# Kernel tuning notes

Measured on AMD Instinct MI355X. Metric: run time of the kernel, lower is better.

## Reference

```python
import jax, jax.numpy as jnp
import numpy as np

B, T, C = 4, 2048, 2048
H, HKV, D = 16, 8, 128
SECTIONS = (24, 20, 20)  # sums to 64 = D/2 -> full-dim rotation branch
EPS = 1e-6


def setup_inputs() -> dict:
    key = jax.random.key(0)
    ks = jax.random.split(key, 8)
    x = jax.random.normal(ks[0], (B, T, C), dtype=jnp.float32)
    # realistic RoPE tables: [3, B, T, 64] (3 mRoPE axes: t/h/w)
    half = sum(SECTIONS)  # 64
    inv_freq = 1.0 / (10000.0 ** (jnp.arange(half, dtype=jnp.float32) / half))
    pos = jnp.arange(T, dtype=jnp.float32)
    freqs = pos[:, None] * inv_freq[None, :]                      # [T, 64]
    freqs3 = jnp.broadcast_to(freqs, (3, B, T, half))
    # small per-axis offsets so the three mRoPE axes differ
    axis_off = jnp.arange(3, dtype=jnp.float32)[:, None, None, None] * 0.5
    cos = jnp.cos(freqs3 + axis_off)
    sin = jnp.sin(freqs3 + axis_off)
    mask = jnp.ones((B, T), dtype=jnp.int32)
    s = 1.0 / np.sqrt(C)
    Wq = jax.random.normal(ks[1], (C, H * D), dtype=jnp.float32) * s
    Wk = jax.random.normal(ks[2], (C, HKV * D), dtype=jnp.float32) * s
    Wv = jax.random.normal(ks[3], (C, HKV * D), dtype=jnp.float32) * s
    Wo = jax.random.normal(ks[4], (H * D, C), dtype=jnp.float32) * (1.0 / np.sqrt(H * D))
    return dict(x=x, cos=cos, sin=sin, mask=mask,
                Wq=Wq, bq=jnp.zeros((H * D,), jnp.float32),
                Wk=Wk, bk=jnp.zeros((HKV * D,), jnp.float32),
                Wv=Wv, bv=jnp.zeros((HKV * D,), jnp.float32),
                gq=jnp.ones((D,), jnp.float32), gk=jnp.ones((D,), jnp.float32),
                Wo=Wo)


def _rms_norm(x, gamma, eps):
    var = jnp.mean(jnp.square(x.astype(jnp.float32)), axis=-1, keepdims=True)
    return (gamma * x * jax.lax.rsqrt(var + eps)).astype(x.dtype)


def _rotate_half(x):
    x1, x2 = jnp.split(x, 2, axis=-1)
    return jnp.concatenate((-x2, x1), axis=-1)


def _reorder(table):
    # interleave mRoPE sections: take section i from axis i, then duplicate
    chunks, off = [], 0
    for i, sec in enumerate(SECTIONS):
        chunks.append(table[i, ..., off:off + sec])
        off += sec
    r = jnp.concatenate(chunks, axis=-1)        # [B, T, 64]
    return jnp.concatenate([r, r], axis=-1)     # [B, T, 128]


def reference(x, cos, sin, mask, Wq, bq, Wk, bk, Wv, bv, gq, gk, Wo):
    b, t = x.shape[0], x.shape[1]
    q = (x @ Wq + bq).reshape(b, t, H, D)
    k = (x @ Wk + bk).reshape(b, t, HKV, D)
    v = (x @ Wv + bv).reshape(b, t, HKV, D)
    q = _rms_norm(q, gq, EPS)
    k = _rms_norm(k, gk, EPS)
    q = jnp.transpose(q, (0, 2, 1, 3))   # [B, H, T, D]
    k = jnp.transpose(k, (0, 2, 1, 3))   # [B, HKV, T, D]
    v = jnp.transpose(v, (0, 2, 1, 3))
    cos_e = _reorder(cos)[:, None].astype(q.dtype)  # [B, 1, T, D]
    sin_e = _reorder(sin)[:, None].astype(q.dtype)
    q = q * cos_e + _rotate_half(q) * sin_e
    k = k * cos_e + _rotate_half(k) * sin_e
    key_mask = mask.astype(jnp.float32)                         # [B, T]
    lengths = key_mask.sum(axis=-1).astype(jnp.int32)           # [B]
    k = k * key_mask[:, None, :, None].astype(k.dtype)
    v = v * key_mask[:, None, :, None].astype(v.dtype)
    history_mask = (jnp.arange(t)[None, :] < lengths[:, None]).astype(jnp.float32)
    repeats = H // HKV
    qg = q.reshape(b, HKV, repeats, t, D)
    scores = jnp.einsum('bhgqd,bhkd->bhgqk', qg.astype(jnp.float32),
                        k.astype(jnp.float32)) * D ** -0.5
    scores = scores.reshape(b, H, t, t)
    scores = scores + (1.0 - history_mask)[:, None, None, :] * -1e9
    causal = jnp.tril(jnp.ones((t, t), dtype=jnp.float32))
    scores = scores + (1.0 - causal)[None, None] * -1e9
    weights = jax.nn.softmax(scores, axis=-1)
    wg = weights.reshape(b, HKV, repeats, t, t)
    out = jnp.einsum('bhgqk,bhkd->bhgqd', wg, v.astype(jnp.float32))
    out = out.reshape(b, H, t, D).astype(x.dtype)
    out = jnp.transpose(out, (0, 2, 1, 3)).reshape(b, t, H * D)
    return out @ Wo
```

## Files before the change

### kernel.cpp

```cpp
#include <hip/hip_runtime.h>
#include <stdint.h>

#define B_    4
#define T_    2048
#define C_    2048
#define H_    16
#define HKV_  8
#define D_    128
#define HD_   2048
#define KVD_  1024
#define NQKV_ 4096
#define BT_   8192

typedef __bf16 bf16x8 __attribute__((ext_vector_type(8)));
typedef float  f32x4  __attribute__((ext_vector_type(4)));
typedef unsigned short u16;
typedef unsigned int   u32;

__device__ __forceinline__ u16 f2b(float f){
  union { float f; u32 u; } v; v.f = f;
  u32 r = v.u + 0x7FFFu + ((v.u >> 16) & 1u);
  return (u16)(r >> 16);
}
__device__ __forceinline__ float b2f(u16 h){
  union { u32 u; float f; } v; v.u = ((u32)h) << 16;
  return v.f;
}

#define GLOAD16(src, dst) __builtin_amdgcn_global_load_lds( \
    (const __attribute__((address_space(1))) u32*)(src), \
    (__attribute__((address_space(3))) u32*)(dst), 16, 0, 0)

#define MFMA16(a,b,c) __builtin_amdgcn_mfma_f32_16x16x32_bf16((a), (b), (c), 0, 0, 0)

__global__ __launch_bounds__(256) void k_misc(const float* __restrict__ x, u16* __restrict__ xb,
                                              const float* __restrict__ bq, const float* __restrict__ bk,
                                              const float* __restrict__ bv, float* __restrict__ bias,
                                              const int* __restrict__ mask, int* __restrict__ lens){
  int bid = blockIdx.x;
  if (bid < 16384){
    size_t i = ((size_t)bid * 256 + threadIdx.x) * 4;
    float4 v = *(const float4*)(x + i);
    u32 w0 = (u32)f2b(v.x) | ((u32)f2b(v.y) << 16);
    u32 w1 = (u32)f2b(v.z) | ((u32)f2b(v.w) << 16);
    uint2 pk; pk.x = w0; pk.y = w1;
    *(uint2*)(xb + i) = pk;
  } else if (bid < 16400){
    int i = (bid - 16384) * 256 + threadIdx.x;
    if (i < NQKV_)
      bias[i] = (i < HD_) ? bq[i] : (i < HD_ + KVD_ ? bk[i - HD_] : bv[i - HD_ - KVD_]);
  } else {
    int b = bid - 16400;
    int s = 0;
    for (int t = threadIdx.x; t < T_; t += 256) s += mask[b * T_ + t];
    #pragma unroll
    for (int d = 1; d < 64; d <<= 1) s += __shfl_xor(s, d);
    __shared__ int acc[4];
    if ((threadIdx.x & 63) == 0) acc[threadIdx.x >> 6] = s;
    __syncthreads();
    if (threadIdx.x == 0) lens[b] = acc[0] + acc[1] + acc[2] + acc[3];
  }
}

__global__ __launch_bounds__(256) void k_wtrans(const float* __restrict__ Wq, const float* __restrict__ Wk,
                                                const float* __restrict__ Wv, const float* __restrict__ Wo,
                                                u16* __restrict__ WQKVT, u16* __restrict__ WOT){
  int z = blockIdx.z;
  const float* src; u16* dst; int N;
  if (z == 0){ src = Wq; dst = WQKVT;                          N = 2048; }
  else if (z == 1){ src = Wo; dst = WOT;                       N = 2048; }
  else if (z == 2){ src = Wk; dst = WQKVT + (size_t)HD_ * C_;  N = 1024; }
  else { src = Wv; dst = WQKVT + (size_t)(HD_ + KVD_) * C_;    N = 1024; }
  if (blockIdx.x * 64 >= N) return;
  const int K = 2048;
  __shared__ __attribute__((aligned(16))) u16 tile[64][68];
  int n0 = blockIdx.x * 64, k0 = blockIdx.y * 64;
  int r = threadIdx.x >> 4, c4 = (threadIdx.x & 15) * 4;
  #pragma unroll
  for (int rr = 0; rr < 4; ++rr){
    int kl = r + rr * 16;
    float4 v = *(const float4*)(src + (size_t)(k0 + kl) * N + n0 + c4);
    tile[kl][c4+0] = f2b(v.x); tile[kl][c4+1] = f2b(v.y);
    tile[kl][c4+2] = f2b(v.z); tile[kl][c4+3] = f2b(v.w);
  }
  __syncthreads();
  #pragma unroll
  for (int rr = 0; rr < 4; ++rr){
    int nl = r + rr * 16;
    u32 w0 = (u32)tile[c4+0][nl] | ((u32)tile[c4+1][nl] << 16);
    u32 w1 = (u32)tile[c4+2][nl] | ((u32)tile[c4+3][nl] << 16);
    uint2 pk; pk.x = w0; pk.y = w1;
    *(uint2*)(dst + (size_t)(n0 + nl) * K + k0 + c4) = pk;
  }
}

template<bool OUTF32>
__global__ __launch_bounds__(512, 2) void k_gemm(const u16* __restrict__ A, const u16* __restrict__ BT,
                                                 const float* __restrict__ bias, void* __restrict__ Cout,
                                                 int M, int N, int K, int nbx){
  __shared__ __attribute__((aligned(16))) u16 As[2][256 * 64];
  __shared__ __attribute__((aligned(16))) u16 Bs[2][256 * 64];
  int nwg = gridDim.x;
  int fid = blockIdx.x;
  int gs = (fid & 7) * (nwg >> 3) + (fid >> 3);
  int bx = gs % nbx, by = gs / nbx;
  int m0 = by * 256, n0 = bx * 256;
  int tid = threadIdx.x;
  int lane = tid & 63, w = tid >> 6;
  int wm = w >> 2, wn = w & 3;
  int g = lane >> 4, lo = lane & 15;
  int lsx = (lo & 7) << 3;
  int wgb = tid & 448;
  f32x4 acc[8][4] = {};

  auto STAGE_HALF = [&](const u16* __restrict__ src, int k0, u16* lds){
    #pragma unroll
    for (int i = 0; i < 2; ++i){
      int gI = i * 512 + tid;
      int row = gI >> 3, grp = gI & 7;
      GLOAD16(src + (size_t)row * K + k0 + ((grp ^ (row & 7)) << 3),
              &lds[(i * 512 + wgb) * 8]);
    }
  };
  auto STAGE_TILE = [&](int k0, int bufi){
    STAGE_HALF(A  + (size_t)m0 * K,          k0, &As[bufi][0]);
    STAGE_HALF(A  + (size_t)(m0 + 128) * K,  k0, &As[bufi][8192]);
    STAGE_HALF(BT + (size_t)n0 * K,          k0, &Bs[bufi][0]);
    STAGE_HALF(BT + (size_t)(n0 + 128) * K,  k0, &Bs[bufi][8192]);
  };

  int nk = K >> 6;
  STAGE_TILE(0, 0);
  for (int t = 0; t < nk; ++t){
    int cur = t & 1, nxt = cur ^ 1;
    bool pf = (t + 1 < nk);
    if (pf){
      STAGE_TILE((t + 1) * 64, nxt);
      asm volatile("s_waitcnt vmcnt(8)" ::: "memory");
    } else {
      asm volatile("s_waitcnt vmcnt(0)" ::: "memory");
    }
    __builtin_amdgcn_s_barrier();
    __builtin_amdgcn_sched_barrier(0);
    bf16x8 bfr[4][2];
    #pragma unroll
    for (int nr = 0; nr < 4; ++nr){
      bfr[nr][0] = *(const bf16x8*)&Bs[cur][(wn*64 + nr*16 + lo) * 64 + ((0*32 + g*8) ^ lsx)];
      bfr[nr][1] = *(const bf16x8*)&Bs[cur][(wn*64 + nr*16 + lo) * 64 + ((1*32 + g*8) ^ lsx)];
    }
    __builtin_amdgcn_s_setprio(1);
    #pragma unroll
    for (int p = 0; p < 4; ++p){
      int r0 = 2 * p, r1 = 2 * p + 1;
      bf16x8 a00 = *(const bf16x8*)&As[cur][(wm*128 + r0*16 + lo) * 64 + ((0*32 + g*8) ^ lsx)];
      bf16x8 a01 = *(const bf16x8*)&As[cur][(wm*128 + r0*16 + lo) * 64 + ((1*32 + g*8) ^ lsx)];
      bf16x8 a10 = *(const bf16x8*)&As[cur][(wm*128 + r1*16 + lo) * 64 + ((0*32 + g*8) ^ lsx)];
      bf16x8 a11 = *(const bf16x8*)&As[cur][(wm*128 + r1*16 + lo) * 64 + ((1*32 + g*8) ^ lsx)];
      #pragma unroll
      for (int nr = 0; nr < 4; ++nr){
        acc[r0][nr] = MFMA16(a00, bfr[nr][0], acc[r0][nr]);
        acc[r0][nr] = MFMA16(a01, bfr[nr][1], acc[r0][nr]);
        acc[r1][nr] = MFMA16(a10, bfr[nr][0], acc[r1][nr]);
        acc[r1][nr] = MFMA16(a11, bfr[nr][1], acc[r1][nr]);
      }
    }
    __builtin_amdgcn_s_setprio(0);
    __builtin_amdgcn_s_barrier();
  }
  #pragma unroll
  for (int mr = 0; mr < 8; ++mr){
    #pragma unroll
    for (int nr = 0; nr < 4; ++nr){
      #pragma unroll
      for (int r = 0; r < 4; ++r){
        int row = m0 + wm*128 + mr*16 + g*4 + r;
        int col = n0 + wn*64 + nr*16 + lo;
        float v = acc[mr][nr][r] + (bias ? bias[col] : 0.0f);
        if (OUTF32) ((float*)Cout)[(size_t)row * N + col] = v;
        else        ((u16*)Cout)[(size_t)row * N + col] = f2b(v);
      }
    }
  }
}

__global__ __launch_bounds__(256) void k_post(const u16* __restrict__ qkv,
    const float* __restrict__ cosp, const float* __restrict__ sinp,
    const int* __restrict__ mask, const float* __restrict__ gq, const float* __restrict__ gk,
    u16* __restrict__ qrot, u16* __restrict__ krot, u16* __restrict__ vt){
  int bid = blockIdx.x;
  if (bid < BT_){
    const float QS = 0.08838834764831845f * 1.4426950408889634f;
    int tok = bid;
    int b = tok >> 11, t = tok & (T_ - 1);
    int lane = threadIdx.x & 63, w = threadIdx.x >> 6;
    int dl = (lane & 31) * 2;
    int a0 = dl < 24 ? 0 : (dl < 44 ? 1 : 2);
    int a1 = (dl + 1) < 24 ? 0 : ((dl + 1) < 44 ? 1 : 2);
    size_t cb = ((size_t)b * T_ + t) * 64;
    const size_t AX = (size_t)B_ * T_ * 64;
    float ce0 = cosp[(size_t)a0 * AX + cb + dl],     se0 = sinp[(size_t)a0 * AX + cb + dl];
    float ce1 = cosp[(size_t)a1 * AX + cb + dl + 1], se1 = sinp[(size_t)a1 * AX + cb + dl + 1];
    float sgn = (lane < 32) ? -1.f : 1.f;
    float mk = (float)mask[b * T_ + t];
    const u16* base = qkv + (size_t)tok * NQKV_;
    for (int head = w; head < H_ + HKV_; head += 4){
      bool isq = head < H_;
      int off = isq ? head * D_ : HD_ + (head - H_) * D_;
      u32 pr = *(const u32*)(base + off + lane * 2);
      float x0 = b2f((u16)(pr & 0xFFFF)), x1 = b2f((u16)(pr >> 16));
      float ss = x0*x0 + x1*x1;
      #pragma unroll
      for (int d = 1; d < 64; d <<= 1) ss += __shfl_xor(ss, d);
      float rinv = rsqrtf(ss * (1.0f / 128.0f) + 1e-6f);
      const float* gg = isq ? gq : gk;
      float2 gv = *(const float2*)(gg + lane * 2);
      float n0 = gv.x * x0 * rinv, n1 = gv.y * x1 * rinv;
      float p0 = __shfl_xor(n0, 32), p1 = __shfl_xor(n1, 32);
      float o0 = n0 * ce0 + sgn * p0 * se0;
      float o1 = n1 * ce1 + sgn * p1 * se1;
      u16* dst;
      if (isq){
        o0 *= QS; o1 *= QS;
        dst = qrot + ((size_t)(b * H_ + head) * T_ + t) * D_;
      } else {
        o0 *= mk; o1 *= mk;
        dst = krot + ((size_t)(b * HKV_ + (head - H_)) * T_ + t) * D_;
      }
      u32 ow = (u32)f2b(o0) | ((u32)f2b(o1) << 16);
      *(u32*)(dst + lane * 2) = ow;
    }
  } else {
    int bid2 = bid - BT_;
    int t0 = (bid2 & 31) * 64, d0 = ((bid2 >> 5) & 1) * 64;
    int bh = bid2 >> 6;
    int b = bh >> 3, hk = bh & 7;
    __shared__ __attribute__((aligned(16))) u16 tile[64][68];
    int r = threadIdx.x >> 4, c4 = (threadIdx.x & 15) * 4;
    #pragma unroll
    for (int rr = 0; rr < 4; ++rr){
      int tl = r + rr * 16;
      int t = t0 + tl;
      u16 mz = (u16)(mask[b * T_ + t] ? 0xFFFFu : 0u);
      ushort4 v = *(const ushort4*)(qkv + (size_t)(b * T_ + t) * NQKV_ + HD_ + KVD_ + hk * D_ + d0 + c4);
      tile[tl][c4+0] = (u16)(v.x & mz); tile[tl][c4+1] = (u16)(v.y & mz);
      tile[tl][c4+2] = (u16)(v.z & mz); tile[tl][c4+3] = (u16)(v.w & mz);
    }
    __syncthreads();
    #pragma unroll
    for (int rr = 0; rr < 4; ++rr){
      int dn = r + rr * 16;
      u32 w0 = (u32)tile[c4+0][dn] | ((u32)tile[c4+1][dn] << 16);
      u32 w1 = (u32)tile[c4+2][dn] | ((u32)tile[c4+3][dn] << 16);
      uint2 pk; pk.x = w0; pk.y = w1;
      *(uint2*)(vt + ((size_t)bh * D_ + d0 + dn) * T_ + t0 + c4) = pk;
    }
  }
}

__global__ __launch_bounds__(512) void k_attn(const u16* __restrict__ qrot, const u16* __restrict__ krot,
                                              const u16* __restrict__ vt, const int* __restrict__ lens,
                                              u16* __restrict__ ao){
  int fid = blockIdx.x;
  int gs = (fid & 7) * 128 + (fid >> 3);
  int qi = (gs & 15) ^ 15;
  int q0 = qi * 128;
  int h = (gs >> 4) & 15, b = gs >> 8;
  int hk = h >> 1;
  int tid = threadIdx.x;
  int lane = tid & 63, w = tid >> 6;
  int g = lane >> 4, lo = lane & 15;
  int len = lens[b];
  __shared__ __attribute__((aligned(16))) u16 Ks[2][64 * 128];
  __shared__ __attribute__((aligned(16))) u16 Vs[2][128 * 64];
  const u16* qbase = qrot + ((size_t)(b * H_ + h) * T_ + q0 + w * 16 + lo) * D_ + g * 8;
  bf16x8 qf[4];
  #pragma unroll
  for (int kk = 0; kk < 4; ++kk) qf[kk] = *(const bf16x8*)(qbase + kk * 32);
  float m_run = -1e30f, l_run = 0.f;
  f32x4 o[8] = {};
  int qrow = q0 + w * 16 + lo;
  const u16* kbase = krot + (size_t)(b * HKV_ + hk) * T_ * D_;
  const u16* vbase = vt   + (size_t)(b * HKV_ + hk) * D_ * T_;
  int wbase = tid & 448;
  int lsx = (lo & 7) << 3;
  int srcA = ((lane & 16) * 2 + lo) * 4;
  int srcB = srcA + 64;
  bool hiL = lane >= 32;

  auto STAGE = [&](int j0, int bufi){
    #pragma unroll
    for (int i = 0; i < 2; ++i){
      int gI = i * 512 + tid;
      int row = gI >> 4, grp = gI & 15;
      GLOAD16(kbase + (size_t)(j0 + row) * D_ + ((grp ^ (row & 7)) << 3),
              &Ks[bufi][(i * 512 + wbase) * 8]);
    }
    #pragma unroll
    for (int i = 0; i < 2; ++i){
      int gI = i * 512 + tid;
      int row = gI >> 3, grp = gI & 7;
      GLOAD16(vbase + (size_t)row * T_ + j0 + ((grp ^ (row & 7)) << 3),
              &Vs[bufi][(i * 512 + wbase) * 8]);
    }
  };

  STAGE(0, 0);
  int cur = 0;
  int jend = q0 + 64;
  for (int j0 = 0; j0 <= jend && j0 < len; j0 += 64){
    int jn = j0 + 64;
    bool hasnext = (jn <= jend && jn < len);
    if (hasnext){
      STAGE(jn, cur ^ 1);
      asm volatile("s_waitcnt vmcnt(4)" ::: "memory");
    } else {
      asm volatile("s_waitcnt vmcnt(0)" ::: "memory");
    }
    __builtin_amdgcn_s_barrier();
    __builtin_amdgcn_sched_barrier(0);
    bool wlive = (j0 <= q0 + w * 16 + 15);
    if (wlive){
      f32x4 st[4] = {};
      __builtin_amdgcn_s_setprio(1);
      #pragma unroll
      for (int kk = 0; kk < 4; ++kk){
        #pragma unroll
        for (int nf = 0; nf < 4; ++nf){
          bf16x8 kf = *(const bf16x8*)&Ks[cur][(nf * 16 + lo) * 128 + ((kk * 32 + g * 8) ^ lsx)];
          st[nf] = MFMA16(kf, qf[kk], st[nf]);
        }
      }
      __builtin_amdgcn_s_setprio(0);
      bool needmask = (j0 + 63 > q0 + w * 16) || (j0 + 64 > len);
      if (needmask){
        #pragma unroll
        for (int nf = 0; nf < 4; ++nf)
          #pragma unroll
          for (int r = 0; r < 4; ++r){
            int k = j0 + nf * 16 + g * 4 + r;
            if (k > qrow || k >= len) st[nf][r] = -1e30f;
          }
      }
      float mf[4];
      #pragma unroll
      for (int nf = 0; nf < 4; ++nf)
        mf[nf] = fmaxf(fmaxf(st[nf][0], st[nf][1]), fmaxf(st[nf][2], st[nf][3]));
      float mx = fmaxf(fmaxf(mf[0], mf[1]), fmaxf(mf[2], mf[3]));
      mx = fmaxf(mx, __shfl_xor(mx, 16));
      mx = fmaxf(mx, __shfl_xor(mx, 32));
      bool skip = __all(mx <= m_run + 8.0f);
      float mn = skip ? m_run : fmaxf(m_run, mx);
      float sf[4];
      #pragma unroll
      for (int nf = 0; nf < 4; ++nf){
        #pragma unroll
        for (int r = 0; r < 4; ++r){
          float e = exp2f(st[nf][r] - mn);
          st[nf][r] = e;
        }
        sf[nf] = (st[nf][0] + st[nf][1]) + (st[nf][2] + st[nf][3]);
      }
      float sum = (sf[0] + sf[1]) + (sf[2] + sf[3]);
      sum += __shfl_xor(sum, 16);
      sum += __shfl_xor(sum, 32);
      if (skip){
        l_run += sum;
      } else {
        float alpha = exp2f(m_run - mn);
        l_run = l_run * alpha + sum;
        m_run = mn;
        #pragma unroll
        for (int r = 0; r < 4; ++r){
          float ar = __shfl(alpha, (lane & 48) | ((g * 4 + r) & 15));
          #pragma unroll
          for (int df = 0; df < 8; ++df) o[df][r] *= ar;
        }
      }
      u32 pk[4][2];
      #pragma unroll
      for (int nf = 0; nf < 4; ++nf){
        union { u32 u; __bf16 hh[2]; } c0, c1;
        c0.hh[0] = (__bf16)st[nf][0]; c0.hh[1] = (__bf16)st[nf][1];
        c1.hh[0] = (__bf16)st[nf][2]; c1.hh[1] = (__bf16)st[nf][3];
        pk[nf][0] = c0.u; pk[nf][1] = c1.u;
      }
      #pragma unroll
      for (int kk2 = 0; kk2 < 2; ++kk2){
        u32 a0 = (u32)__builtin_amdgcn_ds_bpermute(srcA, (int)pk[2*kk2][0]);
        u32 b0 = (u32)__builtin_amdgcn_ds_bpermute(srcA, (int)pk[2*kk2+1][0]);
        u32 a1 = (u32)__builtin_amdgcn_ds_bpermute(srcA, (int)pk[2*kk2][1]);
        u32 b1 = (u32)__builtin_amdgcn_ds_bpermute(srcA, (int)pk[2*kk2+1][1]);
        u32 a2 = (u32)__builtin_amdgcn_ds_bpermute(srcB, (int)pk[2*kk2][0]);
        u32 b2 = (u32)__builtin_amdgcn_ds_bpermute(srcB, (int)pk[2*kk2+1][0]);
        u32 a3 = (u32)__builtin_amdgcn_ds_bpermute(srcB, (int)pk[2*kk2][1]);
        u32 b3 = (u32)__builtin_amdgcn_ds_bpermute(srcB, (int)pk[2*kk2+1][1]);
        union { u32 u[4]; bf16x8 v; } pf;
        pf.u[0] = hiL ? b0 : a0;
        pf.u[1] = hiL ? b1 : a1;
        pf.u[2] = hiL ? b2 : a2;
        pf.u[3] = hiL ? b3 : a3;
        __builtin_amdgcn_s_setprio(1);
        #pragma unroll
        for (int df = 0; df < 8; ++df){
          bf16x8 vf = *(const bf16x8*)&Vs[cur][(df * 16 + lo) * 64 + ((kk2 * 32 + g * 8) ^ lsx)];
          o[df] = MFMA16(pf.v, vf, o[df]);
        }
        __builtin_amdgcn_s_setprio(0);
      }
    }
    __builtin_amdgcn_s_barrier();
    cur ^= 1;
  }
  #pragma unroll
  for (int r = 0; r < 4; ++r){
    float lr = __shfl(l_run, (lane & 48) | ((g * 4 + r) & 15));
    float rl = 1.0f / lr;
    int row = q0 + w * 16 + g * 4 + r;
    #pragma unroll
    for (int df = 0; df < 8; ++df){
      float ov = o[df][r] * rl;
      ao[((size_t)(b * T_ + row)) * HD_ + h * D_ + df * 16 + lo] = f2b(ov);
    }
  }
}

extern "C" void kernel_launch(void* const* d_in, const int* in_sizes, int n_in,
                              void* d_out, int out_size, void* d_ws, size_t ws_size,
                              hipStream_t stream) {
  (void)in_sizes; (void)n_in; (void)out_size; (void)ws_size;
  const float* x    = (const float*)d_in[0];
  const float* cosp = (const float*)d_in[1];
  const float* sinp = (const float*)d_in[2];
  const int*   mask = (const int*)d_in[3];
  const float* Wq   = (const float*)d_in[4];
  const float* bq   = (const float*)d_in[5];
  const float* Wk   = (const float*)d_in[6];
  const float* bk   = (const float*)d_in[7];
  const float* Wv   = (const float*)d_in[8];
  const float* bv   = (const float*)d_in[9];
  const float* gq   = (const float*)d_in[10];
  const float* gk   = (const float*)d_in[11];
  const float* Wo   = (const float*)d_in[12];

  char* ws = (char*)d_ws;
  const size_t MB = 1024 * 1024;
  u16*   XB    = (u16*)(ws);
  u16*   WQKVT = (u16*)(ws + 32  * MB);
  u16*   WOT   = (u16*)(ws + 48  * MB);
  u16*   QKV   = (u16*)(ws + 56  * MB);
  u16*   QROT  = (u16*)(ws + 120 * MB);
  u16*   KROT  = (u16*)(ws + 152 * MB);
  u16*   VT    = (u16*)(ws + 168 * MB);
  u16*   AO    = (u16*)(ws + 184 * MB);
  float* BIAS  = (float*)(ws + 216 * MB);
  int*   LENS  = (int*)(ws + 216 * MB + 65536);

  k_misc<<<16404, 256, 0, stream>>>(x, XB, bq, bk, bv, BIAS, mask, LENS);
  k_wtrans<<<dim3(32, 32, 4), 256, 0, stream>>>(Wq, Wk, Wv, Wo, WQKVT, WOT);

  k_gemm<false><<<512, 512, 0, stream>>>(XB, WQKVT, BIAS, QKV, BT_, NQKV_, C_, 16);
  k_post<<<BT_ + 2048, 256, 0, stream>>>(QKV, cosp, sinp, mask, gq, gk, QROT, KROT, VT);
  k_attn<<<1024, 512, 0, stream>>>(QROT, KROT, VT, LENS, AO);
  k_gemm<true><<<256, 512, 0, stream>>>(AO, WOT, nullptr, d_out, BT_, C_, HD_, 8);
}
```

Measured before the change: 479.4 us.

## Shrink GEMM tiles to 128x256 with BK=32 for higher occupancy

Reworks the bf16 MFMA GEMM from 256x256 tiles with a K-step of 64 to 128x256 tiles with a K-step of 32. Shared memory per block drops to 48KB and the accumulator array halves, so launch bounds are raised to allow four blocks per CU, and both grids are doubled to match. The aim is better latency hiding and more blocks to cover the CUs. In exchange, each LDS byte is reused less, barriers come twice as often per unit of K, and A/B traffic from global memory rises.

```diff
diff --git a/kernel.cpp b/kernel.cpp
--- a/kernel.cpp
+++ b/kernel.cpp
@@ -95,86 +95,78 @@
 }
 
 template<bool OUTF32>
-__global__ __launch_bounds__(512, 2) void k_gemm(const u16* __restrict__ A, const u16* __restrict__ BT,
+__global__ __launch_bounds__(512, 4) void k_gemm(const u16* __restrict__ A, const u16* __restrict__ BT,
                                                  const float* __restrict__ bias, void* __restrict__ Cout,
                                                  int M, int N, int K, int nbx){
-  __shared__ __attribute__((aligned(16))) u16 As[2][256 * 64];
-  __shared__ __attribute__((aligned(16))) u16 Bs[2][256 * 64];
+  __shared__ __attribute__((aligned(16))) u16 As[2][128 * 32];
+  __shared__ __attribute__((aligned(16))) u16 Bs[2][256 * 32];
   int nwg = gridDim.x;
   int fid = blockIdx.x;
   int gs = (fid & 7) * (nwg >> 3) + (fid >> 3);
   int bx = gs % nbx, by = gs / nbx;
-  int m0 = by * 256, n0 = bx * 256;
+  int m0 = by * 128, n0 = bx * 256;
   int tid = threadIdx.x;
   int lane = tid & 63, w = tid >> 6;
   int wm = w >> 2, wn = w & 3;
   int g = lane >> 4, lo = lane & 15;
-  int lsx = (lo & 7) << 3;
-  int wgb = tid & 448;
-  f32x4 acc[8][4] = {};
-
-  auto STAGE_HALF = [&](const u16* __restrict__ src, int k0, u16* lds){
+  f32x4 acc[4][4] = {};
+
+  auto STAGE_TILE = [&](int k0, int bufi){
+    {
+      int row = tid >> 2, gr = tid & 3;
+      GLOAD16(A + (size_t)(m0 + row) * K + k0 + ((gr ^ ((row >> 1) & 3)) << 3),
+              &As[bufi][(tid & 448) * 8]);
+    }
     #pragma unroll
     for (int i = 0; i < 2; ++i){
       int gI = i * 512 + tid;
-      int row = gI >> 3, grp = gI & 7;
-      GLOAD16(src + (size_t)row * K + k0 + ((grp ^ (row & 7)) << 3),
-              &lds[(i * 512 + wgb) * 8]);
+      int row = gI >> 2, gr = gI & 3;
+      GLOAD16(BT + (size_t)(n0 + row) * K + k0 + ((gr ^ ((row >> 1) & 3)) << 3),
+              &Bs[bufi][(i * 512 + (tid & 448)) * 8]);
     }
   };
-  auto STAGE_TILE = [&](int k0, int bufi){
-    STAGE_HALF(A  + (size_t)m0 * K,          k0, &As[bufi][0]);
-    STAGE_HALF(A  + (size_t)(m0 + 128) * K,  k0, &As[bufi][8192]);
-    STAGE_HALF(BT + (size_t)n0 * K,          k0, &Bs[bufi][0]);
-    STAGE_HALF(BT + (size_t)(n0 + 128) * K,  k0, &Bs[bufi][8192]);
-  };
-
-  int nk = K >> 6;
+
+  int nk = K >> 5;
   STAGE_TILE(0, 0);
   for (int t = 0; t < nk; ++t){
     int cur = t & 1, nxt = cur ^ 1;
     bool pf = (t + 1 < nk);
     if (pf){
-      STAGE_TILE((t + 1) * 64, nxt);
-      asm volatile("s_waitcnt vmcnt(8)" ::: "memory");
+      STAGE_TILE((t + 1) * 32, nxt);
+      asm volatile("s_waitcnt vmcnt(3)" ::: "memory");
     } else {
       asm volatile("s_waitcnt vmcnt(0)" ::: "memory");
     }
     __builtin_amdgcn_s_barrier();
     __builtin_amdgcn_sched_barrier(0);
-    bf16x8 bfr[4][2];
+    bf16x8 bfr[4], af[4];
     #pragma unroll
     for (int nr = 0; nr < 4; ++nr){
-      bfr[nr][0] = *(const bf16x8*)&Bs[cur][(wn*64 + nr*16 + lo) * 64 + ((0*32 + g*8) ^ lsx)];
-      bfr[nr][1] = *(const bf16x8*)&Bs[cur][(wn*64 + nr*16 + lo) * 64 + ((1*32 + g*8) ^ lsx)];
+      int brow = wn * 64 + nr * 16 + lo;
+      bfr[nr] = *(const bf16x8*)&Bs[cur][brow * 32 + ((g ^ ((brow >> 1) & 3)) << 3)];
+    }
+    #pragma unroll
+    for (int mr = 0; mr < 4; ++mr){
+      int arow = wm * 64 + mr * 16 + lo;
+      af[mr] = *(const bf16x8*)&As[cur][arow * 32 + ((g ^ ((arow >> 1) & 3)) << 3)];
     }
     __builtin_amdgcn_s_setprio(1);
     #pragma unroll
-    for (int p = 0; p < 4; ++p){
-      int r0 = 2 * p, r1 = 2 * p + 1;
-      bf16x8 a00 = *(const bf16x8*)&As[cur][(wm*128 + r0*16 + lo) * 64 + ((0*32 + g*8) ^ lsx)];
-      bf16x8 a01 = *(const bf16x8*)&As[cur][(wm*128 + r0*16 + lo) * 64 + ((1*32 + g*8) ^ lsx)];
-      bf16x8 a10 = *(const bf16x8*)&As[cur][(wm*128 + r1*16 + lo) * 64 + ((0*32 + g*8) ^ lsx)];
-      bf16x8 a11 = *(const bf16x8*)&As[cur][(wm*128 + r1*16 + lo) * 64 + ((1*32 + g*8) ^ lsx)];
-      #pragma unroll
-      for (int nr = 0; nr < 4; ++nr){
-        acc[r0][nr] = MFMA16(a00, bfr[nr][0], acc[r0][nr]);
-        acc[r0][nr] = MFMA16(a01, bfr[nr][1], acc[r0][nr]);
-        acc[r1][nr] = MFMA16(a10, bfr[nr][0], acc[r1][nr]);
-        acc[r1][nr] = MFMA16(a11, bfr[nr][1], acc[r1][nr]);
-      }
-    }
+    for (int mr = 0; mr < 4; ++mr)
+      #pragma unroll
+      for (int nr = 0; nr < 4; ++nr)
+        acc[mr][nr] = MFMA16(af[mr], bfr[nr], acc[mr][nr]);
     __builtin_amdgcn_s_setprio(0);
     __builtin_amdgcn_s_barrier();
   }
   #pragma unroll
-  for (int mr = 0; mr < 8; ++mr){
+  for (int mr = 0; mr < 4; ++mr){
     #pragma unroll
     for (int nr = 0; nr < 4; ++nr){
       #pragma unroll
       for (int r = 0; r < 4; ++r){
-        int row = m0 + wm*128 + mr*16 + g*4 + r;
-        int col = n0 + wn*64 + nr*16 + lo;
+        int row = m0 + wm * 64 + mr * 16 + g * 4 + r;
+        int col = n0 + wn * 64 + nr * 16 + lo;
         float v = acc[mr][nr][r] + (bias ? bias[col] : 0.0f);
         if (OUTF32) ((float*)Cout)[(size_t)row * N + col] = v;
         else        ((u16*)Cout)[(size_t)row * N + col] = f2b(v);
@@ -458,8 +450,8 @@
   k_misc<<<16404, 256, 0, stream>>>(x, XB, bq, bk, bv, BIAS, mask, LENS);
   k_wtrans<<<dim3(32, 32, 4), 256, 0, stream>>>(Wq, Wk, Wv, Wo, WQKVT, WOT);
 
-  k_gemm<false><<<512, 512, 0, stream>>>(XB, WQKVT, BIAS, QKV, BT_, NQKV_, C_, 16);
+  k_gemm<false><<<1024, 512, 0, stream>>>(XB, WQKVT, BIAS, QKV, BT_, NQKV_, C_, 16);
   k_post<<<BT_ + 2048, 256, 0, stream>>>(QKV, cosp, sinp, mask, gq, gk, QROT, KROT, VT);
   k_attn<<<1024, 512, 0, stream>>>(QROT, KROT, VT, LENS, AO);
-  k_gemm<true><<<256, 512, 0, stream>>>(AO, WOT, nullptr, d_out, BT_, C_, HD_, 8);
-}
+  k_gemm<true><<<512, 512, 0, stream>>>(AO, WOT, nullptr, d_out, BT_, C_, HD_, 8);
+}
```

Result: no change. 479.4 us (+0.0%).
